# Kernel tuning notes

Measured on AMD Instinct MI355X. Metric: run time of the kernel, lower is better.

Reference implementation:

```python
import jax, jax.numpy as jnp
import numpy as np
from jax import lax

D_MODEL = 200
N_LAYER = 12
NHEADS = 8
HEADDIM = 50
D_STATE = 64
D_INNER = 2 * D_MODEL            # 400
CONV_DIM = D_INNER + 2 * D_STATE  # 528 (ngroups=1)
D_IN_PROJ = 2 * D_INNER + 2 * D_STATE + NHEADS  # 936
D_CONV = 4
EPS = 1e-5


def rmsnorm(x, w):
    v = jnp.mean(jnp.square(x), axis=-1, keepdims=True)
    return x * lax.rsqrt(v + EPS) * w


def groupnorm(x, groups, g, b):
    B, C, H, W = x.shape
    xg = x.reshape(B, groups, C // groups, H, W)
    mu = jnp.mean(xg, axis=(2, 3, 4), keepdims=True)
    var = jnp.mean(jnp.square(xg - mu), axis=(2, 3, 4), keepdims=True)
    xn = ((xg - mu) * lax.rsqrt(var + EPS)).reshape(B, C, H, W)
    return xn * g[:, None, None] + b[:, None, None]


def patch_embed(x, pe_conv_w, proj_in_w, gn_g, gn_b, spec_w):
    b, c, l, d = x.shape
    # time path: 'b c l d' -> (b, 1, c*l, d), conv -> (b, 25, c*l, 8)
    time_x = x.reshape(b, 1, c * l, d)
    t = lax.conv_general_dilated(time_x, proj_in_w, (1, 25), ((0, 0), (24, 24)),
                                 dimension_numbers=('NCHW', 'OIHW', 'NCHW'))
    t = jax.nn.gelu(groupnorm(t, 5, gn_g, gn_b), approximate=False)
    time_emb = t.transpose(0, 2, 1, 3).reshape(b, c, l, D_MODEL)
    # freq path: rfft over patch dim, norm='forward'
    spec = jnp.abs(jnp.fft.rfft(x, axis=-1, norm='forward'))  # (b,c,l,101)
    spec_emb = jnp.einsum('bclf,df->bcld', spec, spec_w)
    patch = time_emb + spec_emb
    # depthwise 7x7 positional conv over (d, c, l)
    pos = lax.conv_general_dilated(patch.transpose(0, 3, 1, 2), pe_conv_w, (1, 1),
                                   ((3, 3), (3, 3)),
                                   dimension_numbers=('NCHW', 'OIHW', 'NCHW'),
                                   feature_group_count=D_MODEL)
    return patch + pos.transpose(0, 2, 3, 1)


def ssd_scan(xh, dt, B, C, A, D):
    # xh: (b,l,h,p)  dt: (b,l,h)  B,C: (b,l,n)  A,D: (h,)
    b, l, h, p = xh.shape

    def step(state, inp):
        x_t, dt_t, B_t, C_t = inp
        dA = jnp.exp(dt_t * A)  # (b,h)
        state = state * dA[:, :, None, None] + \
            (dt_t[:, :, None, None] * x_t[:, :, :, None]) * B_t[:, None, None, :]
        y = jnp.einsum('bhpn,bn->bhp', state, C_t)
        return state, y

    state0 = jnp.zeros((b, h, p, D_STATE), xh.dtype)
    _, ys = lax.scan(step, state0,
                     (xh.transpose(1, 0, 2, 3), dt.transpose(1, 0, 2),
                      B.transpose(1, 0, 2), C.transpose(1, 0, 2)))
    return ys.transpose(1, 0, 2, 3) + xh * D[None, None, :, None]


def mamba2(u, in_w, conv_w, conv_b, dt_bias, A_log, D, gn_w, out_w):
    b, l, _ = u.shape
    zxbcdt = u @ in_w.T  # (b,l,936)
    z = zxbcdt[..., :D_INNER]
    xBC = zxbcdt[..., D_INNER:D_INNER + CONV_DIM]
    dt = jax.nn.softplus(zxbcdt[..., D_INNER + CONV_DIM:] + dt_bias)  # (b,l,8)
    # causal depthwise conv1d, kernel 4
    xc = lax.conv_general_dilated(xBC.transpose(0, 2, 1), conv_w, (1,), ((D_CONV - 1, 0),),
                                  dimension_numbers=('NCH', 'OIH', 'NCH'),
                                  feature_group_count=CONV_DIM)
    xBC = jax.nn.silu((xc + conv_b[:, None]).transpose(0, 2, 1))
    x = xBC[..., :D_INNER].reshape(b, l, NHEADS, HEADDIM)
    Bm = xBC[..., D_INNER:D_INNER + D_STATE]
    Cm = xBC[..., D_INNER + D_STATE:]
    y = ssd_scan(x, dt, Bm, Cm, -jnp.exp(A_log), D).reshape(b, l, D_INNER)
    y = rmsnorm(y * jax.nn.silu(z), gn_w)  # RMSNormGated, norm_before_gate=False
    return y @ out_w.T


@jax.checkpoint
def layer(hidden, residual, norm_w, in_w, conv_w, conv_b, dt_bias, A_log, D, gn_w, out_w):
    residual = hidden + residual
    hidden = mamba2(rmsnorm(residual, norm_w), in_w, conv_w, conv_b, dt_bias, A_log, D, gn_w, out_w)
    return hidden, residual


def forward(x, pe_conv_w, proj_in_w, gn_g, gn_b, spec_w, norm_w, in_proj_w, conv_w, conv_b,
            dt_bias, A_log, D, gnorm_w, out_proj_w, norm_f_w, head_w, head_b):
    b, c, l, d = x.shape
    hidden = patch_embed(x, pe_conv_w, proj_in_w, gn_g, gn_b, spec_w).reshape(b, c * l, d)
    residual = jnp.zeros_like(hidden)
    for i in range(N_LAYER):
        hidden, residual = layer(hidden, residual, norm_w[i], in_proj_w[i], conv_w[i],
                                 conv_b[i], dt_bias[i], A_log[i], D[i], gnorm_w[i], out_proj_w[i])
    hidden = rmsnorm(hidden + residual, norm_f_w).reshape(b, c, l, d)
    return hidden @ head_w.T + head_b


def setup_inputs():
    key = jax.random.key(0)
    ks = jax.random.split(key, 12)
    B, CH, L, P = 16, 19, 30, 200

    def g(k, shape, scale):
        return jax.random.normal(k, shape, jnp.float32) * scale

    dt = jax.random.uniform(ks[8], (N_LAYER, NHEADS), jnp.float32, 1e-3, 0.1)
    return {
        'x': g(ks[0], (B, CH, L, P), 1.0),
        'pe_conv_w': g(ks[1], (D_MODEL, 1, 7, 7), 0.15),
        'proj_in_w': g(ks[2], (25, 1, 1, 49), 0.14),
        'gn_g': jnp.ones(25, jnp.float32),
        'gn_b': jnp.zeros(25, jnp.float32),
        'spec_w': g(ks[3], (D_MODEL, 101), 0.1),
        'norm_w': jnp.ones((N_LAYER, D_MODEL), jnp.float32),
        'in_proj_w': g(ks[4], (N_LAYER, D_IN_PROJ, D_MODEL), 0.07),
        'conv_w': g(ks[5], (N_LAYER, CONV_DIM, 1, D_CONV), 0.4),
        'conv_b': jnp.zeros((N_LAYER, CONV_DIM), jnp.float32),
        'dt_bias': jnp.log(jnp.expm1(dt)),
        'A_log': jnp.log(jax.random.uniform(ks[9], (N_LAYER, NHEADS), jnp.float32, 1.0, 16.0)),
        'D': jnp.ones((N_LAYER, NHEADS), jnp.float32),
        'gnorm_w': jnp.ones((N_LAYER, D_INNER), jnp.float32),
        'out_proj_w': g(ks[6], (N_LAYER, D_MODEL, D_INNER), 0.05),
        'norm_f_w': jnp.ones(D_MODEL, jnp.float32),
        'head_w': g(ks[7], (D_MODEL, D_MODEL), 0.07),
        'head_b': jnp.zeros(D_MODEL, jnp.float32),
    }


def reference(x, pe_conv_w, proj_in_w, gn_g, gn_b, spec_w, norm_w, in_proj_w, conv_w, conv_b,
              dt_bias, A_log, D, gnorm_w, out_proj_w, norm_f_w, head_w, head_b):
    return forward(x, pe_conv_w, proj_in_w, gn_g, gn_b, spec_w, norm_w, in_proj_w, conv_w,
                   conv_b, dt_bias, A_log, D, gnorm_w, out_proj_w, norm_f_w, head_w, head_b)
```

## Files before the change

### kernel.cpp

```cpp
#include <hip/hip_runtime.h>
#include <hip/hip_bf16.h>
#include <math.h>

#define D_MODEL   200
#define N_LAYER   12
#define NHEADS    8
#define HEADDIM   50
#define D_STATE   64
#define D_INNER   400
#define CONV_DIM  528
#define D_IN_PROJ 936
#define D_CONV    4
#define EPS       1e-5f

#define BATCH 16
#define CH    19
#define LLEN  30
#define SEQ   570
#define NTOK  9120
#define NFREQ 101

typedef __attribute__((ext_vector_type(8))) short s8v;
typedef __attribute__((ext_vector_type(4))) float f32x4;

__device__ __forceinline__ short f2bf(float f) {
    unsigned u = __float_as_uint(f);
    u += 0x7FFFu + ((u >> 16) & 1u);
    return (short)(u >> 16);
}

__global__ __launch_bounds__(256) void gemm_bf16(
    const short* __restrict__ A, const short* __restrict__ W,
    const float* __restrict__ bias, float* __restrict__ C,
    int M, int N, int Kp, int accum)
{
    __shared__ __align__(16) short As[128][40];
    __shared__ __align__(16) short Ws[128][40];

    int bm = blockIdx.y * 128;
    int bn = blockIdx.x * 128;
    int tid = threadIdx.x;
    int lane = tid & 63;
    int wv = tid >> 6;
    int wm = wv & 1, wn = wv >> 1;
    int lm = lane & 15, lg = lane >> 4;

    int sr = tid >> 1;
    int sh_ = (tid & 1) * 16;

    f32x4 acc[4][4];
#pragma unroll
    for (int i = 0; i < 4; i++)
#pragma unroll
        for (int j = 0; j < 4; j++) acc[i][j] = (f32x4)0.f;

    for (int k0 = 0; k0 < Kp; k0 += 32) {
        {
            s8v v0 = (s8v)0, v1 = (s8v)0;
            if (bm + sr < M) {
                const short* ga = A + (size_t)(bm + sr) * Kp + k0 + sh_;
                v0 = *(const s8v*)ga;
                v1 = *(const s8v*)(ga + 8);
            }
            *(s8v*)&As[sr][sh_] = v0;
            *(s8v*)&As[sr][sh_ + 8] = v1;
        }
        {
            s8v v0 = (s8v)0, v1 = (s8v)0;
            if (bn + sr < N) {
                const short* gw = W + (size_t)(bn + sr) * Kp + k0 + sh_;
                v0 = *(const s8v*)gw;
                v1 = *(const s8v*)(gw + 8);
            }
            *(s8v*)&Ws[sr][sh_] = v0;
            *(s8v*)&Ws[sr][sh_ + 8] = v1;
        }
        __syncthreads();

        s8v af[4], bf[4];
#pragma unroll
        for (int i = 0; i < 4; i++)
            af[i] = *(const s8v*)&As[wm * 64 + i * 16 + lm][lg * 8];
#pragma unroll
        for (int j = 0; j < 4; j++)
            bf[j] = *(const s8v*)&Ws[wn * 64 + j * 16 + lm][lg * 8];
#pragma unroll
        for (int i = 0; i < 4; i++)
#pragma unroll
            for (int j = 0; j < 4; j++)
                acc[i][j] = __builtin_amdgcn_mfma_f32_16x16x32_bf16(
                    af[i], bf[j], acc[i][j], 0, 0, 0);
        __syncthreads();
    }

#pragma unroll
    for (int j = 0; j < 4; j++) {
        int n = bn + wn * 64 + j * 16 + lm;
        if (n >= N) continue;
        float bv = bias ? bias[n] : 0.f;
#pragma unroll
        for (int i = 0; i < 4; i++) {
            int mbase = bm + wm * 64 + i * 16 + lg * 4;
#pragma unroll
            for (int r = 0; r < 4; r++) {
                int m = mbase + r;
                if (m >= M) continue;
                size_t idx = (size_t)m * N + n;
                float v = acc[i][j][r] + bv;
                if (accum) v += C[idx];
                C[idx] = v;
            }
        }
    }
}

__global__ __launch_bounds__(256) void gemm_nt(
    const float* __restrict__ A, const float* __restrict__ W,
    const float* __restrict__ bias, float* __restrict__ C,
    int M, int N, int K, int accum)
{
    const int BM = 128, BK = 16;
    __shared__ float As[16][BM + 4];
    __shared__ float Ws[16][BM + 4];

    int bm = blockIdx.y * BM;
    int bn = blockIdx.x * BM;
    int tid = threadIdx.x;
    int lr = tid >> 1;
    int lc = (tid & 1) * 8;
    int tx = tid & 15;
    int ty = tid >> 4;

    float acc[8][8];
#pragma unroll
    for (int i = 0; i < 8; i++)
#pragma unroll
        for (int j = 0; j < 8; j++) acc[i][j] = 0.f;

    for (int k0 = 0; k0 < K; k0 += BK) {
#pragma unroll
        for (int i = 0; i < 8; i++) {
            int gr = bm + lr, gk = k0 + lc + i;
            As[lc + i][lr] = (gr < M && gk < K) ? A[(size_t)gr * K + gk] : 0.f;
        }
#pragma unroll
        for (int i = 0; i < 8; i++) {
            int gr = bn + lr, gk = k0 + lc + i;
            Ws[lc + i][lr] = (gr < N && gk < K) ? W[(size_t)gr * K + gk] : 0.f;
        }
        __syncthreads();
#pragma unroll
        for (int kk = 0; kk < BK; kk++) {
            float a[8], bv[8];
#pragma unroll
            for (int i = 0; i < 8; i++) a[i] = As[kk][ty * 8 + i];
#pragma unroll
            for (int j = 0; j < 8; j++) bv[j] = Ws[kk][tx * 8 + j];
#pragma unroll
            for (int i = 0; i < 8; i++)
#pragma unroll
                for (int j = 0; j < 8; j++)
                    acc[i][j] = fmaf(a[i], bv[j], acc[i][j]);
        }
        __syncthreads();
    }

#pragma unroll
    for (int i = 0; i < 8; i++) {
        int gm = bm + ty * 8 + i;
        if (gm >= M) continue;
#pragma unroll
        for (int j = 0; j < 8; j++) {
            int gn = bn + tx * 8 + j;
            if (gn >= N) continue;
            float v = acc[i][j];
            if (bias) v += bias[gn];
            if (accum) v += C[(size_t)gm * N + gn];
            C[(size_t)gm * N + gn] = v;
        }
    }
}

__global__ __launch_bounds__(256) void cast_pad_kernel(
    const float* __restrict__ src, short* __restrict__ dst,
    int R, int K, int Kp)
{
    int idx = blockIdx.x * 256 + threadIdx.x;
    if (idx >= R * Kp) return;
    int r = idx / Kp, k = idx - r * Kp;
    dst[idx] = (k < K) ? f2bf(src[(size_t)r * K + k]) : (short)0;
}

__global__ __launch_bounds__(256) void time_conv_kernel(
    const float* __restrict__ x, const float* __restrict__ pw,
    float* __restrict__ traw)
{
    int br = blockIdx.x;
    __shared__ float xr[200];
    if (threadIdx.x < 200) xr[threadIdx.x] = x[(size_t)br * 200 + threadIdx.x];
    __syncthreads();
    if (threadIdx.x < 200) {
        int oc = threadIdx.x >> 3, j = threadIdx.x & 7;
        int start = j * 25 - 24;
        float acc = 0.f;
#pragma unroll
        for (int k = 0; k < 49; k++) {
            int d = start + k;
            if (d >= 0 && d < 200) acc = fmaf(xr[d], pw[oc * 49 + k], acc);
        }
        int b = br / SEQ, row = br % SEQ;
        traw[(((size_t)b * 25 + oc) * SEQ + row) * 8 + j] = acc;
    }
}

__global__ __launch_bounds__(256) void gn_stats_kernel(
    const float* __restrict__ traw, float* __restrict__ stats)
{
    int bg = blockIdx.x;
    int b = bg / 5, g = bg % 5;
    const float* base = traw + ((size_t)b * 25 + g * 5) * SEQ * 8;
    float s = 0.f, q = 0.f;
    for (int i = threadIdx.x; i < 5 * SEQ * 8; i += 256) {
        float v = base[i];
        s += v; q = fmaf(v, v, q);
    }
    __shared__ float rs[4], rq[4];
    int lane = threadIdx.x & 63, w = threadIdx.x >> 6;
#pragma unroll
    for (int o = 32; o; o >>= 1) { s += __shfl_xor(s, o, 64); q += __shfl_xor(q, o, 64); }
    if (lane == 0) { rs[w] = s; rq[w] = q; }
    __syncthreads();
    if (threadIdx.x == 0) {
        float S = rs[0] + rs[1] + rs[2] + rs[3];
        float Q = rq[0] + rq[1] + rq[2] + rq[3];
        float inv = 1.f / (5.f * SEQ * 8.f);
        float mean = S * inv;
        float var = Q * inv - mean * mean;
        stats[bg * 2] = mean;
        stats[bg * 2 + 1] = rsqrtf(var + EPS);
    }
}

__global__ __launch_bounds__(256) void gn_gelu_kernel(
    const float* __restrict__ traw, const float* __restrict__ stats,
    const float* __restrict__ gn_g, const float* __restrict__ gn_b,
    float* __restrict__ patch)
{
    int idx = blockIdx.x * 256 + threadIdx.x;
    if (idx >= NTOK * 200) return;
    int d = idx % 200;
    int row = (idx / 200) % SEQ;
    int b = idx / (200 * SEQ);
    int oc = d >> 3, j = d & 7;
    float v = traw[(((size_t)b * 25 + oc) * SEQ + row) * 8 + j];
    int g = oc / 5;
    float mean = stats[(b * 5 + g) * 2];
    float rstd = stats[(b * 5 + g) * 2 + 1];
    v = (v - mean) * rstd * gn_g[oc] + gn_b[oc];
    float ge = 0.5f * v * (1.f + erff(v * 0.70710678118654752f));
    patch[idx] = ge;
}
// ... 275 lines not shown
                tok = (tid >= 66) ? 1 : 0;
                fidx = tid - tok * 66;
                int tq = t + 2 + tok; if (tq > SEQ - 1) tq = SEQ - 1;
                int g = (fidx < 50) ? (50 * bz + fidx) : (fidx + 50);
                rx = ((const float4*)(xBC + (size_t)(b * SEQ + tq) * CONV_DIM))[g];
            } else if (tid < 140) {
                int e = tid - 132, tk = e >> 2, hd = e & 3;
                int tq = t + 2 + tk; if (tq > SEQ - 1) tq = SEQ - 1;
                rdt = dtb[(size_t)(b * SEQ + tq) * NHEADS + bz * 4 + hd];
            }
        }
#pragma unroll
        for (int k = 0; k < 2; k++) {
            float dtv = sh[buf][k][264 + hl];
            float xp  = (p < HEADDIM) ? sh[buf][k][hl * HEADDIM + p] : 0.f;
            float dA = __expf(dtv * A);
            float u  = dtv * xp;
            pacc *= dA;
            const float4* B4 = (const float4*)&sh[buf][k][200];
#pragma unroll
            for (int n4 = 0; n4 < 16; n4++) {
                float4 bq = B4[n4];
                s[4 * n4 + 0] = fmaf(s[4 * n4 + 0], dA, u * bq.x);
                s[4 * n4 + 1] = fmaf(s[4 * n4 + 1], dA, u * bq.y);
                s[4 * n4 + 2] = fmaf(s[4 * n4 + 2], dA, u * bq.z);
                s[4 * n4 + 3] = fmaf(s[4 * n4 + 3], dA, u * bq.w);
            }
        }
        if (pf) {
            if (tid < 132) *(float4*)&sh[nb][tok][fidx * 4] = rx;
            else if (tid < 140) { int e = tid - 132; sh[nb][e >> 2][264 + (e & 3)] = rdt; }
        }
        __syncthreads();
    }

    if (rem) {
        int buf = npairs & 1;
        float dtv = sh[buf][0][264 + hl];
        float xp  = (p < HEADDIM) ? sh[buf][0][hl * HEADDIM + p] : 0.f;
        float dA = __expf(dtv * A);
        float u  = dtv * xp;
        pacc *= dA;
        const float4* B4 = (const float4*)&sh[buf][0][200];
#pragma unroll
        for (int n4 = 0; n4 < 16; n4++) {
            float4 bq = B4[n4];
            s[4 * n4 + 0] = fmaf(s[4 * n4 + 0], dA, u * bq.x);
            s[4 * n4 + 1] = fmaf(s[4 * n4 + 1], dA, u * bq.y);
            s[4 * n4 + 2] = fmaf(s[4 * n4 + 2], dA, u * bq.z);
            s[4 * n4 + 3] = fmaf(s[4 * n4 + 3], dA, u * bq.w);
        }
    }

    if (p < HEADDIM) {
        float* Sb = Sbuf + ((size_t)((b * NHEADS + h) * nchunk + c)) * (HEADDIM * 64)
                    + p * 64;
#pragma unroll
        for (int n4 = 0; n4 < 16; n4++)
            ((float4*)Sb)[n4] = make_float4(s[4 * n4], s[4 * n4 + 1],
                                            s[4 * n4 + 2], s[4 * n4 + 3]);
    }
    if (p == 0) Pd[(b * NHEADS + h) * nchunk + c] = pacc;
}

__global__ __launch_bounds__(512) void ssd_state_kernel(
    const float* __restrict__ xBC, const float* __restrict__ dtb,
    const float* __restrict__ A_log, float* __restrict__ Sbuf,
    float* __restrict__ Pd, int layer, int lchunk, int nchunk)
{
    int b = blockIdx.x, c = blockIdx.y;
    int tid = threadIdx.x;
    int h = tid >> 6, p = tid & 63;
    float A = -expf(A_log[layer * NHEADS + h]);

    __shared__ float sh[2][544];
    int t0 = c * lchunk, tend = t0 + lchunk;

    {
        const float* base = xBC + (size_t)(b * SEQ + t0) * CONV_DIM;
        sh[0][tid] = base[tid];
        if (tid < 24) {
            int e2 = 512 + tid;
            sh[0][e2] = (e2 < 528) ? base[e2]
                                   : dtb[(size_t)(b * SEQ + t0) * NHEADS + (e2 - 528)];
        }
    }
    __syncthreads();

    float s[64];
#pragma unroll
    for (int n = 0; n < 64; n++) s[n] = 0.f;
    float pacc = 1.f;

    for (int t = t0; t < tend; t++) {
        int cur = (t - t0) & 1, nxt = cur ^ 1;
        float pf0 = 0.f, pf1 = 0.f;
        if (t + 1 < tend) {
            const float* base = xBC + (size_t)(b * SEQ + t + 1) * CONV_DIM;
            pf0 = base[tid];
            if (tid < 24) {
                int e2 = 512 + tid;
                pf1 = (e2 < 528) ? base[e2]
                                 : dtb[(size_t)(b * SEQ + t + 1) * NHEADS + (e2 - 528)];
            }
        }
        float dtv = sh[cur][528 + h];
        float xp  = (p < HEADDIM) ? sh[cur][h * HEADDIM + p] : 0.f;
        float dA = __expf(dtv * A);
        float u  = dtv * xp;
        pacc *= dA;
        const float4* B4 = (const float4*)&sh[cur][D_INNER];
#pragma unroll
        for (int n4 = 0; n4 < 16; n4++) {
            float4 bq = B4[n4];
            s[4 * n4 + 0] = fmaf(s[4 * n4 + 0], dA, u * bq.x);
            s[4 * n4 + 1] = fmaf(s[4 * n4 + 1], dA, u * bq.y);
            s[4 * n4 + 2] = fmaf(s[4 * n4 + 2], dA, u * bq.z);
            s[4 * n4 + 3] = fmaf(s[4 * n4 + 3], dA, u * bq.w);
        }
        if (t + 1 < tend) {
            sh[nxt][tid] = pf0;
            if (tid < 24) sh[nxt][512 + tid] = pf1;
        }
        __syncthreads();
    }

    if (p < HEADDIM) {
        float* Sb = Sbuf + ((size_t)((b * NHEADS + h) * nchunk + c)) * (HEADDIM * 64)
                    + p * 64;
#pragma unroll
        for (int n4 = 0; n4 < 16; n4++)
            ((float4*)Sb)[n4] = make_float4(s[4 * n4], s[4 * n4 + 1],
                                            s[4 * n4 + 2], s[4 * n4 + 3]);
    }
    if (p == 0) Pd[(b * NHEADS + h) * nchunk + c] = pacc;
}

__global__ __launch_bounds__(256) void ssd_scan2b_kernel(
    float* __restrict__ Sbuf, const float* __restrict__ Pd, int nchunk)
{
    int bh = blockIdx.x;
    int e = blockIdx.y * 256 + threadIdx.x;
    if (e >= HEADDIM * 64) return;
    float* base = Sbuf + (size_t)bh * nchunk * (HEADDIM * 64) + e;
    const float* pd = Pd + bh * nchunk;
    float cur = 0.f;
    for (int c = 0; c < nchunk; c++) {
        float l = base[(size_t)c * (HEADDIM * 64)];
        base[(size_t)c * (HEADDIM * 64)] = cur;
        cur = fmaf(pd[c], cur, l);
    }
}

__global__ __launch_bounds__(512) void ssd_out_fused3_kernel(
    const float* __restrict__ xBC, const float* __restrict__ dtb,
    const float* __restrict__ zxbcdt, const float* __restrict__ A_log,
    const float* __restrict__ Dv, const float* __restrict__ Sbuf,
    const float* __restrict__ gw, short* __restrict__ ybf,
    int layer, int lchunk, int nchunk)
{
    int b = blockIdx.x, c = blockIdx.y;
    int tid = threadIdx.x;
    int h = tid >> 6, p = tid & 63;
    float A = -expf(A_log[layer * NHEADS + h]);
    float Dh = Dv[layer * NHEADS + h];
    float gval = (p < HEADDIM) ? gw[(size_t)layer * D_INNER + h * HEADDIM + p] : 0.f;

    __shared__ __align__(16) float sh[2][2][536];
    __shared__ __align__(16) float shz[2][2][400];
    __shared__ float red[2][2][8];
    int t0 = c * lchunk;
    int npairs = lchunk >> 1, rem = lchunk & 1;

    {
        if (tid < 264) {
            int wch = (tid >= 132) ? 1 : 0;
            int fidx = tid - wch * 132;
            int tq = t0 + wch;
            float4 v = ((const float4*)(xBC + (size_t)(b * SEQ + tq) * CONV_DIM))[fidx];
            *(float4*)&sh[0][wch][fidx * 4] = v;
        } else if (tid < 280) {
            int e = tid - 264, tok = e >> 3, hd = e & 7;
            sh[0][tok][528 + hd] = dtb[(size_t)(b * SEQ + t0 + tok) * NHEADS + hd];
        } else if (tid < 480) {
            int wch = (tid >= 380) ? 1 : 0;
            int fidx = tid - 280 - wch * 100;
            int tq = t0 + wch;
            float4 v = ((const float4*)(zxbcdt + (size_t)(b * SEQ + tq) * D_IN_PROJ))[fidx];
            *(float4*)&shz[0][wch][fidx * 4] = v;
        }
    }

    float s[64];
    if (p < HEADDIM) {
        const float* Sb = Sbuf + ((size_t)((b * NHEADS + h) * nchunk + c)) * (HEADDIM * 64)
                          + p * 64;
#pragma unroll
        for (int n4 = 0; n4 < 16; n4++) {
            float4 v = ((const float4*)Sb)[n4];
            s[4 * n4] = v.x; s[4 * n4 + 1] = v.y; s[4 * n4 + 2] = v.z; s[4 * n4 + 3] = v.w;
        }
    } else {
#pragma unroll
        for (int n = 0; n < 64; n++) s[n] = 0.f;
    }
    __syncthreads();

    for (int i = 0; i < npairs; i++) {
        int t = t0 + 2 * i;
        int buf = i & 1, nb = buf ^ 1;
        bool pf = (2 * i + 2 < lchunk);
        float4 rx, rz;
        float rdt = 0.f;
        int wch = 0, fidx = 0, zwch = 0, zfidx = 0;
        if (pf) {
            if (tid < 264) {
                wch = (tid >= 132) ? 1 : 0;
                fidx = tid - wch * 132;
                int tq = t + 2 + wch; if (tq > SEQ - 1) tq = SEQ - 1;
                rx = ((const float4*)(xBC + (size_t)(b * SEQ + tq) * CONV_DIM))[fidx];
            } else if (tid < 280) {
                int e = tid - 264, tok = e >> 3, hd = e & 7;
                int tq = t + 2 + tok; if (tq > SEQ - 1) tq = SEQ - 1;
                rdt = dtb[(size_t)(b * SEQ + tq) * NHEADS + hd];
            } else if (tid < 480) {
                zwch = (tid >= 380) ? 1 : 0;
                zfidx = tid - 280 - zwch * 100;
                int tq = t + 2 + zwch; if (tq > SEQ - 1) tq = SEQ - 1;
                rz = ((const float4*)(zxbcdt + (size_t)(b * SEQ + tq) * D_IN_PROJ))[zfidx];
            }
        }
        float g0 = 0.f, g1 = 0.f;
#pragma unroll
        for (int k = 0; k < 2; k++) {
            float dtv = sh[buf][k][528 + h];
            float xp  = (p < HEADDIM) ? sh[buf][k][h * HEADDIM + p] : 0.f;
            float dA = __expf(dtv * A);
            float u  = dtv * xp;
            const float4* B4 = (const float4*)&sh[buf][k][D_INNER];
            const float4* C4 = (const float4*)&sh[buf][k][D_INNER + D_STATE];
            float y0 = 0.f, y1 = 0.f, y2 = 0.f, y3 = 0.f;
#pragma unroll
            for (int n4 = 0; n4 < 16; n4++) {
                float4 bq = B4[n4];
                float4 cq = C4[n4];
                float t0v = fmaf(s[4 * n4 + 0], dA, u * bq.x);
                float t1v = fmaf(s[4 * n4 + 1], dA, u * bq.y);
                float t2v = fmaf(s[4 * n4 + 2], dA, u * bq.z);
                float t3v = fmaf(s[4 * n4 + 3], dA, u * bq.w);
                s[4 * n4 + 0] = t0v; s[4 * n4 + 1] = t1v;
                s[4 * n4 + 2] = t2v; s[4 * n4 + 3] = t3v;
                y0 = fmaf(t0v, cq.x, y0);
                y1 = fmaf(t1v, cq.y, y1);
                y2 = fmaf(t2v, cq.z, y2);
                y3 = fmaf(t3v, cq.w, y3);
            }
            if (p < HEADDIM) {
                float yv = fmaf(xp, Dh, (y0 + y1) + (y2 + y3));
                float zv = shz[buf][k][h * HEADDIM + p];
                float g = yv * (zv / (1.f + __expf(-zv)));
                if (k == 0) g0 = g; else g1 = g;
            }
        }
        float gs0 = g0 * g0, gs1 = g1 * g1;
#pragma unroll
        for (int o = 32; o; o >>= 1) {
            gs0 += __shfl_xor(gs0, o, 64);
            gs1 += __shfl_xor(gs1, o, 64);
        }
        if (p == 0) { red[buf][0][h] = gs0; red[buf][1][h] = gs1; }
        if (pf) {
            if (tid < 264) *(float4*)&sh[nb][wch][fidx * 4] = rx;
            else if (tid < 280) { int e = tid - 264; sh[nb][e >> 3][528 + (e & 7)] = rdt; }
            else if (tid < 480) *(float4*)&shz[nb][zwch][zfidx * 4] = rz;
        }
        __syncthreads();
        float tot0 = (red[buf][0][0] + red[buf][0][1]) + (red[buf][0][2] + red[buf][0][3]) +
                     (red[buf][0][4] + red[buf][0][5]) + (red[buf][0][6] + red[buf][0][7]);
        float tot1 = (red[buf][1][0] + red[buf][1][1]) + (red[buf][1][2] + red[buf][1][3]) +
                     (red[buf][1][4] + red[buf][1][5]) + (red[buf][1][6] + red[buf][1][7]);
        float rstd0 = rsqrtf(tot0 * (1.f / D_INNER) + EPS);
        float rstd1 = rsqrtf(tot1 * (1.f / D_INNER) + EPS);
        size_t row0 = (size_t)(b * SEQ + t) * 416;
        size_t row1 = (size_t)(b * SEQ + t + 1) * 416;
        if (p < HEADDIM) {
            ybf[row0 + h * HEADDIM + p] = f2bf(g0 * rstd0 * gval);
            ybf[row1 + h * HEADDIM + p] = f2bf(g1 * rstd1 * gval);
        } else {
            int widx = h * 14 + (p - HEADDIM);
            if (widx < 16) {
                ybf[row0 + 400 + widx] = 0;
                ybf[row1 + 400 + widx] = 0;
            }
        }
    }

    if (rem) {
        int buf = npairs & 1;
        int t = t0 + lchunk - 1;
        float g0 = 0.f;
        {
            float dtv = sh[buf][0][528 + h];
            float xp  = (p < HEADDIM) ? sh[buf][0][h * HEADDIM + p] : 0.f;
            float dA = __expf(dtv * A);
            float u  = dtv * xp;
            const float4* B4 = (const float4*)&sh[buf][0][D_INNER];
            const float4* C4 = (const float4*)&sh[buf][0][D_INNER + D_STATE];
            float y0 = 0.f, y1 = 0.f, y2 = 0.f, y3 = 0.f;
#pragma unroll
            for (int n4 = 0; n4 < 16; n4++) {
                float4 bq = B4[n4];
                float4 cq = C4[n4];
                float t0v = fmaf(s[4 * n4 + 0], dA, u * bq.x);
                float t1v = fmaf(s[4 * n4 + 1], dA, u * bq.y);
                float t2v = fmaf(s[4 * n4 + 2], dA, u * bq.z);
                float t3v = fmaf(s[4 * n4 + 3], dA, u * bq.w);
                s[4 * n4 + 0] = t0v; s[4 * n4 + 1] = t1v;
                s[4 * n4 + 2] = t2v; s[4 * n4 + 3] = t3v;
                y0 = fmaf(t0v, cq.x, y0);
                y1 = fmaf(t1v, cq.y, y1);
                y2 = fmaf(t2v, cq.z, y2);
                y3 = fmaf(t3v, cq.w, y3);
            }
            if (p < HEADDIM) {
                float yv = fmaf(xp, Dh, (y0 + y1) + (y2 + y3));
                float zv = shz[buf][0][h * HEADDIM + p];
                g0 = yv * (zv / (1.f + __expf(-zv)));
            }
        }
        float gs0 = g0 * g0;
#pragma unroll
        for (int o = 32; o; o >>= 1) gs0 += __shfl_xor(gs0, o, 64);
        if (p == 0) red[buf][0][h] = gs0;
        __syncthreads();
        float tot0 = (red[buf][0][0] + red[buf][0][1]) + (red[buf][0][2] + red[buf][0][3]) +
                     (red[buf][0][4] + red[buf][0][5]) + (red[buf][0][6] + red[buf][0][7]);
        float rstd0 = rsqrtf(tot0 * (1.f / D_INNER) + EPS);
        size_t row0 = (size_t)(b * SEQ + t) * 416;
        if (p < HEADDIM) {
            ybf[row0 + h * HEADDIM + p] = f2bf(g0 * rstd0 * gval);
        } else {
            int widx = h * 14 + (p - HEADDIM);
            if (widx < 16) ybf[row0 + 400 + widx] = 0;
        }
    }
}

__global__ __launch_bounds__(512) void ssd_out_kernel(
    const float* __restrict__ xBC, const float* __restrict__ dtb,
    const float* __restrict__ A_log, const float* __restrict__ Dv,
    const float* __restrict__ Sbuf, float* __restrict__ y,
    int layer, int lchunk, int nchunk)
{
    int b = blockIdx.x, c = blockIdx.y;
    int tid = threadIdx.x;
    int h = tid >> 6, p = tid & 63;
    float A = -expf(A_log[layer * NHEADS + h]);
    float Dh = Dv[layer * NHEADS + h];

    __shared__ float sh[2][544];
    int t0 = c * lchunk, tend = t0 + lchunk;

    {
        const float* base = xBC + (size_t)(b * SEQ + t0) * CONV_DIM;
        sh[0][tid] = base[tid];
        if (tid < 24) {
            int e2 = 512 + tid;
            sh[0][e2] = (e2 < 528) ? base[e2]
                                   : dtb[(size_t)(b * SEQ + t0) * NHEADS + (e2 - 528)];
        }
    }

    float s[64];
    if (p < HEADDIM) {
        const float* Sb = Sbuf + ((size_t)((b * NHEADS + h) * nchunk + c)) * (HEADDIM * 64)
                          + p * 64;
#pragma unroll
        for (int n4 = 0; n4 < 16; n4++) {
            float4 v = ((const float4*)Sb)[n4];
            s[4 * n4] = v.x; s[4 * n4 + 1] = v.y; s[4 * n4 + 2] = v.z; s[4 * n4 + 3] = v.w;
        }
    } else {
#pragma unroll
        for (int n = 0; n < 64; n++) s[n] = 0.f;
    }
    __syncthreads();

    for (int t = t0; t < tend; t++) {
        int cur = (t - t0) & 1, nxt = cur ^ 1;
        float pf0 = 0.f, pf1 = 0.f;
        if (t + 1 < tend) {
            const float* base = xBC + (size_t)(b * SEQ + t + 1) * CONV_DIM;
            pf0 = base[tid];
            if (tid < 24) {
                int e2 = 512 + tid;
                pf1 = (e2 < 528) ? base[e2]
                                 : dtb[(size_t)(b * SEQ + t + 1) * NHEADS + (e2 - 528)];
            }
        }
        float dtv = sh[cur][528 + h];
        float xp  = (p < HEADDIM) ? sh[cur][h * HEADDIM + p] : 0.f;
        float dA = __expf(dtv * A);
        float u  = dtv * xp;
        const float4* B4 = (const float4*)&sh[cur][D_INNER];
        const float4* C4 = (const float4*)&sh[cur][D_INNER + D_STATE];
        float y0 = 0.f, y1 = 0.f, y2 = 0.f, y3 = 0.f;
#pragma unroll
        for (int n4 = 0; n4 < 16; n4++) {
            float4 bq = B4[n4];
            float4 cq = C4[n4];
            float t0v = fmaf(s[4 * n4 + 0], dA, u * bq.x);
            float t1v = fmaf(s[4 * n4 + 1], dA, u * bq.y);
            float t2v = fmaf(s[4 * n4 + 2], dA, u * bq.z);
            float t3v = fmaf(s[4 * n4 + 3], dA, u * bq.w);
            s[4 * n4 + 0] = t0v; s[4 * n4 + 1] = t1v;
            s[4 * n4 + 2] = t2v; s[4 * n4 + 3] = t3v;
            y0 = fmaf(t0v, cq.x, y0);
            y1 = fmaf(t1v, cq.y, y1);
            y2 = fmaf(t2v, cq.z, y2);
            y3 = fmaf(t3v, cq.w, y3);
        }
        if (p < HEADDIM) {
            float yv = (y0 + y1) + (y2 + y3);
            y[(size_t)(b * SEQ + t) * D_INNER + h * HEADDIM + p] = fmaf(xp, Dh, yv);
        }
        if (t + 1 < tend) {
            sh[nxt][tid] = pf0;
            if (tid < 24) sh[nxt][512 + tid] = pf1;
        }
        __syncthreads();
    }
}

__global__ __launch_bounds__(256) void gate_norm_kernel(
    float* __restrict__ y, const float* __restrict__ zxbcdt,
    const float* __restrict__ gw, short* __restrict__ ybf, int layer)
{
    int m = blockIdx.x;
    __shared__ float buf[D_INNER];
    __shared__ float red[4];
    const float* z = zxbcdt + (size_t)m * D_IN_PROJ;
    float* yr = y + (size_t)m * D_INNER;
    const float* gwl = gw + (size_t)layer * D_INNER;
    float ss = 0.f;
    for (int k = threadIdx.x; k < D_INNER; k += 256) {
        float zv = z[k];
        float sz = zv / (1.f + expf(-zv));
        float g = yr[k] * sz;
        buf[k] = g;
        ss = fmaf(g, g, ss);
    }
    int lane = threadIdx.x & 63, w = threadIdx.x >> 6;
#pragma unroll
    for (int o = 32; o; o >>= 1) ss += __shfl_xor(ss, o, 64);
    if (lane == 0) red[w] = ss;
    __syncthreads();
    float tot = red[0] + red[1] + red[2] + red[3];
    float rstd = rsqrtf(tot * (1.f / D_INNER) + EPS);
    for (int k = threadIdx.x; k < 416; k += 256) {
        if (k < D_INNER) {
            float v = buf[k] * rstd * gwl[k];
            yr[k] = v;
            if (ybf) ybf[(size_t)m * 416 + k] = f2bf(v);
        } else if (ybf) {
            ybf[(size_t)m * 416 + k] = 0;
        }
    }
}

extern "C" void kernel_launch(void* const* d_in, const int* in_sizes, int n_in,
                              void* d_out, int out_size, void* d_ws, size_t ws_size,
                              hipStream_t stream)
{
    const float* x         = (const float*)d_in[0];
    const float* pe_conv_w = (const float*)d_in[1];
    const float* proj_in_w = (const float*)d_in[2];
    const float* gn_g      = (const float*)d_in[3];
    const float* gn_b      = (const float*)d_in[4];
    const float* spec_w    = (const float*)d_in[5];
    const float* norm_w    = (const float*)d_in[6];
    const float* in_proj_w = (const float*)d_in[7];
    const float* conv_w    = (const float*)d_in[8];
    const float* conv_b    = (const float*)d_in[9];
    const float* dt_bias   = (const float*)d_in[10];
    const float* A_log     = (const float*)d_in[11];
    const float* Dv        = (const float*)d_in[12];
    const float* gnorm_w   = (const float*)d_in[13];
    const float* out_proj_w= (const float*)d_in[14];
    const float* norm_f_w  = (const float*)d_in[15];
    const float* head_w    = (const float*)d_in[16];
    const float* head_b    = (const float*)d_in[17];
    float* out = (float*)d_out;
    float* ws  = (float*)d_ws;

    const size_t needA = 27929344ull * sizeof(float);
    int fast = (ws_size >= needA) ? 1 : 0;

    int nchunk, lchunk;
    float *residual = ws, *hidden = ws + 1824000;
    float *zxbcdt, *xBC, *dtb, *Sbuf, *Pd;
    float *ubuf = nullptr, *ybuf = nullptr;
    short *w_in_bf = nullptr, *w_out_bf = nullptr, *w_head_bf = nullptr,
          *w_spec_bf = nullptr, *csmat_bf = nullptr, *x_bf = nullptr,
          *ubuf_bf = nullptr, *ybuf_bf = nullptr, *magb_bf = nullptr;

    if (fast) {
        nchunk = 15; lchunk = 38;
        zxbcdt = ws + 3648000;
        xBC    = ws + 12184320;
        dtb    = ws + 16999680;
        Sbuf   = ws + 17072640;
        Pd     = ws + 23216640;
        short* pool = (short*)(ws + 23218560);
        w_in_bf   = pool;
        w_out_bf  = pool + 2515968;
        w_head_bf = pool + 3514368;
        w_spec_bf = pool + 3559168;
        ubuf_bf   = pool + 3584768;
        ybuf_bf   = pool + 5627648;
        csmat_bf  = (short*)(Sbuf + 4000000);
        x_bf      = (short*)(Sbuf + 4100000);
        magb_bf   = (short*)(Sbuf + 5200000);
    } else {
        nchunk = 6; lchunk = 95;
        ubuf   = ws + 3648000;
        zxbcdt = ws + 5472000;
        xBC    = ws + 14008320;
        dtb    = ws + 18823680;
        ybuf   = ws + 18896640;
        Sbuf   = ws + 1824000;
        Pd     = ws + 5470000;
    }

    float* traw  = fast ? Sbuf : ybuf;
    float* patch = zxbcdt;
    float* csout = fast ? (Sbuf + 2000000) : (xBC + 50000);
    float* csmat = xBC;
    float* magb  = fast ? nullptr : (xBC + 2000000);
    float* stats = dtb;

    if (fast) {
        cast_pad_kernel<<<(12 * 936 * 224 + 255) / 256, 256, 0, stream>>>(
            in_proj_w, w_in_bf, 12 * 936, 200, 224);
        cast_pad_kernel<<<(12 * 200 * 416 + 255) / 256, 256, 0, stream>>>(
            out_proj_w, w_out_bf, 12 * 200, 400, 416);
        cast_pad_kernel<<<(200 * 224 + 255) / 256, 256, 0, stream>>>(
            head_w, w_head_bf, 200, 200, 224);
        cast_pad_kernel<<<(200 * 128 + 255) / 256, 256, 0, stream>>>(
            spec_w, w_spec_bf, 200, 101, 128);
        cast_pad_kernel<<<(9120 * 224 + 255) / 256, 256, 0, stream>>>(
            x, x_bf, 9120, 200, 224);
        dft_init_bf_kernel<<<(202 * 224 + 255) / 256, 256, 0, stream>>>(csmat_bf);
    } else {
        dft_init_kernel<<<(202 * 200 + 255) / 256, 256, 0, stream>>>(csmat);
    }

    time_conv_kernel<<<NTOK, 256, 0, stream>>>(x, proj_in_w, traw);
    gn_stats_kernel<<<80, 256, 0, stream>>>(traw, stats);
    gn_gelu_kernel<<<(NTOK * 200 + 255) / 256, 256, 0, stream>>>(traw, stats, gn_g, gn_b, patch);
    if (fast) {
        gemm_bf16<<<dim3(2, 72), 256, 0, stream>>>(x_bf, csmat_bf, nullptr, csout,
                                                   NTOK, 202, 224, 0);
        mag_bf_kernel<<<(NTOK * 128 + 255) / 256, 256, 0, stream>>>(csout, magb_bf);
        gemm_bf16<<<dim3(2, 72), 256, 0, stream>>>(magb_bf, w_spec_bf, nullptr, patch,
                                                   NTOK, 200, 128, 1);
    } else {
        gemm_nt<<<dim3(2, 72), 256, 0, stream>>>(x, csmat, nullptr, csout, NTOK, 202, 200, 0);
        mag_kernel<<<(NTOK * NFREQ + 255) / 256, 256, 0, stream>>>(csout, magb);
        gemm_nt<<<dim3(2, 72), 256, 0, stream>>>(magb, spec_w, nullptr, patch,
                                                 NTOK, 200, NFREQ, 1);
    }
    pe_conv3_kernel<<<dim3(16, 13, 5), 256, 0, stream>>>(patch, pe_conv_w, hidden);

    for (int i = 0; i < N_LAYER; i++) {
        if (fast) {
            norm_dt_kernel<<<NTOK, 256, 0, stream>>>(hidden, residual, norm_w + i * 200,
                                                     ubuf_bf, in_proj_w, dt_bias, dtb,
                                                     i, (i == 0) ? 1 : 0);
            gemm_bf16<<<dim3(8, 72), 256, 0, stream>>>(
                ubuf_bf, w_in_bf + (size_t)i * 936 * 224, nullptr, zxbcdt,
                NTOK, D_IN_PROJ, 224, 0);
        } else {
            add_rmsnorm_kernel<<<NTOK, 64, 0, stream>>>(hidden, residual, norm_w + i * 200,
                                                        ubuf, nullptr, (i == 0) ? 1 : 0);
            dt_gemv_kernel<<<NTOK / 4, 256, 0, stream>>>(ubuf, in_proj_w, dt_bias, dtb, i);
            gemm_nt<<<dim3(8, 72), 256, 0, stream>>>(
                ubuf, in_proj_w + (size_t)i * D_IN_PROJ * 200, nullptr, zxbcdt,
                NTOK, D_IN_PROJ, 200, 0);
        }
        dtconv2_kernel<<<dim3(16, 72), 256, 0, stream>>>(zxbcdt, conv_w, conv_b, xBC, i);
        {
            dim3 g(BATCH, nchunk);
            if (fast) {
                ssd_state4_kernel<<<dim3(BATCH, nchunk, 2), 256, 0, stream>>>(
                    xBC, dtb, A_log, Sbuf, Pd, i, lchunk, nchunk);
                ssd_scan2b_kernel<<<dim3(BATCH * NHEADS, 13), 256, 0, stream>>>(Sbuf, Pd, nchunk);
                ssd_out_fused3_kernel<<<g, 512, 0, stream>>>(
                    xBC, dtb, zxbcdt, A_log, Dv, Sbuf, gnorm_w, ybuf_bf, i, lchunk, nchunk);
                gemm_bf16<<<dim3(2, 72), 256, 0, stream>>>(
                    ybuf_bf, w_out_bf + (size_t)i * 200 * 416, nullptr, hidden,
                    NTOK, 200, 416, 0);
            } else {
                ssd_state_kernel<<<g, 512, 0, stream>>>(xBC, dtb, A_log, Sbuf, Pd,
                                                        i, lchunk, nchunk);
                ssd_scan2b_kernel<<<dim3(BATCH * NHEADS, 13), 256, 0, stream>>>(Sbuf, Pd, nchunk);
                ssd_out_kernel<<<g, 512, 0, stream>>>(xBC, dtb, A_log, Dv, Sbuf, ybuf,
                                                      i, lchunk, nchunk);
                gate_norm_kernel<<<NTOK, 256, 0, stream>>>(ybuf, zxbcdt, gnorm_w, nullptr, i);
                gemm_nt<<<dim3(2, 72), 256, 0, stream>>>(
                    ybuf, out_proj_w + (size_t)i * 200 * D_INNER, nullptr, hidden,
                    NTOK, 200, D_INNER, 0);
            }
        }
    }

    add_rmsnorm_kernel<<<NTOK, 64, 0, stream>>>(hidden, residual, norm_f_w,
                                                fast ? nullptr : ubuf,
                                                fast ? ubuf_bf : nullptr, 0);
    if (fast) {
        gemm_bf16<<<dim3(2, 72), 256, 0, stream>>>(ubuf_bf, w_head_bf, head_b, out,
                                                   NTOK, 200, 224, 0);
    } else {
        gemm_nt<<<dim3(2, 72), 256, 0, stream>>>(ubuf, head_w, head_b, out,
                                                 NTOK, 200, 200, 0);
    }
}
```

Measured before the change: 2.490 ms.

## Split SSD output kernel across head halves and defer group-norm scale to GEMM

The fused SSD output kernel now runs with two blocks per (batch, chunk), each covering 4 heads with 256 threads, which doubles block count for better occupancy. Because a block no longer sees every head, it writes per-half sums of squares. A small rstd kernel combines the halves, and the out-projection GEMM applies the per-row rstd in its epilogue. The odd-length remainder path is dropped, so this assumes lchunk is even. It also adds one extra kernel launch per layer.

```diff
diff --git a/kernel.cpp b/kernel.cpp
--- a/kernel.cpp
+++ b/kernel.cpp
@@ -31,8 +31,8 @@
 
 __global__ __launch_bounds__(256) void gemm_bf16(
     const short* __restrict__ A, const short* __restrict__ W,
-    const float* __restrict__ bias, float* __restrict__ C,
-    int M, int N, int Kp, int accum)
+    const float* __restrict__ bias, const float* __restrict__ rowscale,
+    float* __restrict__ C, int M, int N, int Kp, int accum)
 {
     __shared__ __align__(16) short As[128][40];
     __shared__ __align__(16) short Ws[128][40];
@@ -106,7 +106,9 @@
                 int m = mbase + r;
                 if (m >= M) continue;
                 size_t idx = (size_t)m * N + n;
-                float v = acc[i][j][r] + bv;
+                float v = acc[i][j][r];
+                if (rowscale) v *= rowscale[m];
+                v += bv;
                 if (accum) v += C[idx];
                 C[idx] = v;
             }
@@ -688,42 +690,43 @@
     }
 }
 
-__global__ __launch_bounds__(512) void ssd_out_fused3_kernel(
+__global__ __launch_bounds__(256) void ssd_out5_kernel(
     const float* __restrict__ xBC, const float* __restrict__ dtb,
     const float* __restrict__ zxbcdt, const float* __restrict__ A_log,
     const float* __restrict__ Dv, const float* __restrict__ Sbuf,
     const float* __restrict__ gw, short* __restrict__ ybf,
-    int layer, int lchunk, int nchunk)
-{
-    int b = blockIdx.x, c = blockIdx.y;
+    float* __restrict__ ssq, int layer, int lchunk, int nchunk)
+{
+    int b = blockIdx.x, c = blockIdx.y, bz = blockIdx.z;
     int tid = threadIdx.x;
-    int h = tid >> 6, p = tid & 63;
+    int hl = tid >> 6, p = tid & 63;
+    int h = bz * 4 + hl;
     float A = -expf(A_log[layer * NHEADS + h]);
     float Dh = Dv[layer * NHEADS + h];
     float gval = (p < HEADDIM) ? gw[(size_t)layer * D_INNER + h * HEADDIM + p] : 0.f;
 
-    __shared__ __align__(16) float sh[2][2][536];
-    __shared__ __align__(16) float shz[2][2][400];
-    __shared__ float red[2][2][8];
+    __shared__ __align__(16) float sh[2][2][336];
+    __shared__ __align__(16) float shz[2][2][200];
+    __shared__ float red[2][2][4];
     int t0 = c * lchunk;
-    int npairs = lchunk >> 1, rem = lchunk & 1;
+    int npairs = lchunk >> 1;
 
     {
-        if (tid < 264) {
-            int wch = (tid >= 132) ? 1 : 0;
-            int fidx = tid - wch * 132;
-            int tq = t0 + wch;
-            float4 v = ((const float4*)(xBC + (size_t)(b * SEQ + tq) * CONV_DIM))[fidx];
-            *(float4*)&sh[0][wch][fidx * 4] = v;
-        } else if (tid < 280) {
-            int e = tid - 264, tok = e >> 3, hd = e & 7;
-            sh[0][tok][528 + hd] = dtb[(size_t)(b * SEQ + t0 + tok) * NHEADS + hd];
-        } else if (tid < 480) {
-            int wch = (tid >= 380) ? 1 : 0;
-            int fidx = tid - 280 - wch * 100;
-            int tq = t0 + wch;
-            float4 v = ((const float4*)(zxbcdt + (size_t)(b * SEQ + tq) * D_IN_PROJ))[fidx];
-            *(float4*)&shz[0][wch][fidx * 4] = v;
+        if (tid < 164) {
+            int tok = (tid >= 82) ? 1 : 0;
+            int fidx = tid - tok * 82;
+            int g = (fidx < 50) ? (50 * bz + fidx) : (fidx + 50);
+            float4 v = ((const float4*)(xBC + (size_t)(b * SEQ + t0 + tok) * CONV_DIM))[g];
+            *(float4*)&sh[0][tok][fidx * 4] = v;
+        } else if (tid < 172) {
+            int e = tid - 164, tok = e >> 2, hd = e & 3;
+            sh[0][tok][328 + hd] = dtb[(size_t)(b * SEQ + t0 + tok) * NHEADS + bz * 4 + hd];
+        }
+        if (tid < 100) {
+            int tok = (tid >= 50) ? 1 : 0;
+            int fz = tid - tok * 50;
+            float4 v = ((const float4*)(zxbcdt + (size_t)(b * SEQ + t0 + tok) * D_IN_PROJ))[50 * bz + fz];
+            *(float4*)&shz[0][tok][fz * 4] = v;
         }
     }
 
@@ -748,33 +751,35 @@
         bool pf = (2 * i + 2 < lchunk);
         float4 rx, rz;
         float rdt = 0.f;
-        int wch = 0, fidx = 0, zwch = 0, zfidx = 0;
+        int xtok = 0, xf = 0, ztok = 0, zf = 0;
         if (pf) {
-            if (tid < 264) {
-                wch = (tid >= 132) ? 1 : 0;
-                fidx = tid - wch * 132;
-                int tq = t + 2 + wch; if (tq > SEQ - 1) tq = SEQ - 1;
-                rx = ((const float4*)(xBC + (size_t)(b * SEQ + tq) * CONV_DIM))[fidx];
-            } else if (tid < 280) {
-                int e = tid - 264, tok = e >> 3, hd = e & 7;
-                int tq = t + 2 + tok; if (tq > SEQ - 1) tq = SEQ - 1;
-                rdt = dtb[(size_t)(b * SEQ + tq) * NHEADS + hd];
-            } else if (tid < 480) {
-                zwch = (tid >= 380) ? 1 : 0;
-                zfidx = tid - 280 - zwch * 100;
-                int tq = t + 2 + zwch; if (tq > SEQ - 1) tq = SEQ - 1;
-                rz = ((const float4*)(zxbcdt + (size_t)(b * SEQ + tq) * D_IN_PROJ))[zfidx];
+            if (tid < 164) {
+                xtok = (tid >= 82) ? 1 : 0;
+                xf = tid - xtok * 82;
+                int tq = t + 2 + xtok; if (tq > SEQ - 1) tq = SEQ - 1;
+                int g = (xf < 50) ? (50 * bz + xf) : (xf + 50);
+                rx = ((const float4*)(xBC + (size_t)(b * SEQ + tq) * CONV_DIM))[g];
+            } else if (tid < 172) {
+                int e = tid - 164, tk = e >> 2, hd = e & 3;
+                int tq = t + 2 + tk; if (tq > SEQ - 1) tq = SEQ - 1;
+                rdt = dtb[(size_t)(b * SEQ + tq) * NHEADS + bz * 4 + hd];
+            }
+            if (tid < 100) {
+                ztok = (tid >= 50) ? 1 : 0;
+                zf = tid - ztok * 50;
+                int tq = t + 2 + ztok; if (tq > SEQ - 1) tq = SEQ - 1;
+                rz = ((const float4*)(zxbcdt + (size_t)(b * SEQ + tq) * D_IN_PROJ))[50 * bz + zf];
             }
         }
         float g0 = 0.f, g1 = 0.f;
 #pragma unroll
         for (int k = 0; k < 2; k++) {
-            float dtv = sh[buf][k][528 + h];
-            float xp  = (p < HEADDIM) ? sh[buf][k][h * HEADDIM + p] : 0.f;
+            float dtv = sh[buf][k][328 + hl];
+            float xp  = (p < HEADDIM) ? sh[buf][k][hl * HEADDIM + p] : 0.f;
             float dA = __expf(dtv * A);
             float u  = dtv * xp;
-            const float4* B4 = (const float4*)&sh[buf][k][D_INNER];
-            const float4* C4 = (const float4*)&sh[buf][k][D_INNER + D_STATE];
+            const float4* B4 = (const float4*)&sh[buf][k][200];
+            const float4* C4 = (const float4*)&sh[buf][k][264];
             float y0 = 0.f, y1 = 0.f, y2 = 0.f, y3 = 0.f;
 #pragma unroll
             for (int n4 = 0; n4 < 16; n4++) {
@@ -793,35 +798,16 @@
             }
             if (p < HEADDIM) {
                 float yv = fmaf(xp, Dh, (y0 + y1) + (y2 + y3));
-                float zv = shz[buf][k][h * HEADDIM + p];
+                float zv = shz[buf][k][hl * HEADDIM + p];
                 float g = yv * (zv / (1.f + __expf(-zv)));
                 if (k == 0) g0 = g; else g1 = g;
             }
         }
-        float gs0 = g0 * g0, gs1 = g1 * g1;
-#pragma unroll
-        for (int o = 32; o; o >>= 1) {
-            gs0 += __shfl_xor(gs0, o, 64);
-            gs1 += __shfl_xor(gs1, o, 64);
-        }
-        if (p == 0) { red[buf][0][h] = gs0; red[buf][1][h] = gs1; }
-        if (pf) {
-            if (tid < 264) *(float4*)&sh[nb][wch][fidx * 4] = rx;
-            else if (tid < 280) { int e = tid - 264; sh[nb][e >> 3][528 + (e & 7)] = rdt; }
-            else if (tid < 480) *(float4*)&shz[nb][zwch][zfidx * 4] = rz;
-        }
-        __syncthreads();
-        float tot0 = (red[buf][0][0] + red[buf][0][1]) + (red[buf][0][2] + red[buf][0][3]) +
-                     (red[buf][0][4] + red[buf][0][5]) + (red[buf][0][6] + red[buf][0][7]);
-        float tot1 = (red[buf][1][0] + red[buf][1][1]) + (red[buf][1][2] + red[buf][1][3]) +
-                     (red[buf][1][4] + red[buf][1][5]) + (red[buf][1][6] + red[buf][1][7]);
-        float rstd0 = rsqrtf(tot0 * (1.f / D_INNER) + EPS);
-        float rstd1 = rsqrtf(tot1 * (1.f / D_INNER) + EPS);
         size_t row0 = (size_t)(b * SEQ + t) * 416;
-        size_t row1 = (size_t)(b * SEQ + t + 1) * 416;
+        size_t row1 = row0 + 416;
         if (p < HEADDIM) {
-            ybf[row0 + h * HEADDIM + p] = f2bf(g0 * rstd0 * gval);
-            ybf[row1 + h * HEADDIM + p] = f2bf(g1 * rstd1 * gval);
+            ybf[row0 + h * HEADDIM + p] = f2bf(g0 * gval);
+            ybf[row1 + h * HEADDIM + p] = f2bf(g1 * gval);
         } else {
             int widx = h * 14 + (p - HEADDIM);
             if (widx < 16) {
@@ -829,57 +815,34 @@
                 ybf[row1 + 400 + widx] = 0;
             }
         }
-    }
-
-    if (rem) {
-        int buf = npairs & 1;
-        int t = t0 + lchunk - 1;
-        float g0 = 0.f;
-        {
-            float dtv = sh[buf][0][528 + h];
-            float xp  = (p < HEADDIM) ? sh[buf][0][h * HEADDIM + p] : 0.f;
-            float dA = __expf(dtv * A);
-            float u  = dtv * xp;
-            const float4* B4 = (const float4*)&sh[buf][0][D_INNER];
-            const float4* C4 = (const float4*)&sh[buf][0][D_INNER + D_STATE];
-            float y0 = 0.f, y1 = 0.f, y2 = 0.f, y3 = 0.f;
-#pragma unroll
-            for (int n4 = 0; n4 < 16; n4++) {
-                float4 bq = B4[n4];
-                float4 cq = C4[n4];
-                float t0v = fmaf(s[4 * n4 + 0], dA, u * bq.x);
-                float t1v = fmaf(s[4 * n4 + 1], dA, u * bq.y);
-                float t2v = fmaf(s[4 * n4 + 2], dA, u * bq.z);
-                float t3v = fmaf(s[4 * n4 + 3], dA, u * bq.w);
-                s[4 * n4 + 0] = t0v; s[4 * n4 + 1] = t1v;
-                s[4 * n4 + 2] = t2v; s[4 * n4 + 3] = t3v;
-                y0 = fmaf(t0v, cq.x, y0);
-                y1 = fmaf(t1v, cq.y, y1);
-                y2 = fmaf(t2v, cq.z, y2);
-                y3 = fmaf(t3v, cq.w, y3);
-            }
-            if (p < HEADDIM) {
-                float yv = fmaf(xp, Dh, (y0 + y1) + (y2 + y3));
-                float zv = shz[buf][0][h * HEADDIM + p];
-                g0 = yv * (zv / (1.f + __expf(-zv)));
-            }
-        }
-        float gs0 = g0 * g0;
-#pragma unroll
-        for (int o = 32; o; o >>= 1) gs0 += __shfl_xor(gs0, o, 64);
-        if (p == 0) red[buf][0][h] = gs0;
+        float gs0 = g0 * g0, gs1 = g1 * g1;
+#pragma unroll
+        for (int o = 32; o; o >>= 1) {
+            gs0 += __shfl_xor(gs0, o, 64);
+            gs1 += __shfl_xor(gs1, o, 64);
+        }
+        if (p == 0) { red[buf][0][hl] = gs0; red[buf][1][hl] = gs1; }
+        if (pf) {
+            if (tid < 164) *(float4*)&sh[nb][xtok][xf * 4] = rx;
+            else if (tid < 172) { int e = tid - 164; sh[nb][e >> 2][328 + (e & 3)] = rdt; }
+            if (tid < 100) *(float4*)&shz[nb][ztok][zf * 4] = rz;
+        }
         __syncthreads();
-        float tot0 = (red[buf][0][0] + red[buf][0][1]) + (red[buf][0][2] + red[buf][0][3]) +
-                     (red[buf][0][4] + red[buf][0][5]) + (red[buf][0][6] + red[buf][0][7]);
-        float rstd0 = rsqrtf(tot0 * (1.f / D_INNER) + EPS);
-        size_t row0 = (size_t)(b * SEQ + t) * 416;
-        if (p < HEADDIM) {
-            ybf[row0 + h * HEADDIM + p] = f2bf(g0 * rstd0 * gval);
-        } else {
-            int widx = h * 14 + (p - HEADDIM);
-            if (widx < 16) ybf[row0 + 400 + widx] = 0;
-        }
-    }
+        if (tid == 0) {
+            ssq[(size_t)(b * SEQ + t) * 2 + bz] =
+                (red[buf][0][0] + red[buf][0][1]) + (red[buf][0][2] + red[buf][0][3]);
+            ssq[(size_t)(b * SEQ + t + 1) * 2 + bz] =
+                (red[buf][1][0] + red[buf][1][1]) + (red[buf][1][2] + red[buf][1][3]);
+        }
+    }
+}
+
+__global__ __launch_bounds__(256) void rstd_kernel(
+    const float* __restrict__ ssq, float* __restrict__ rstdb)
+{
+    int m = blockIdx.x * 256 + threadIdx.x;
+    if (m >= NTOK) return;
+    rstdb[m] = rsqrtf((ssq[2 * m] + ssq[2 * m + 1]) * (1.f / D_INNER) + EPS);
 }
 
 __global__ __launch_bounds__(512) void ssd_out_kernel(
@@ -1029,13 +992,13 @@
     float* out = (float*)d_out;
     float* ws  = (float*)d_ws;
 
-    const size_t needA = 27929344ull * sizeof(float);
+    const size_t needA = 27956704ull * sizeof(float);
     int fast = (ws_size >= needA) ? 1 : 0;
 
     int nchunk, lchunk;
     float *residual = ws, *hidden = ws + 1824000;
     float *zxbcdt, *xBC, *dtb, *Sbuf, *Pd;
-    float *ubuf = nullptr, *ybuf = nullptr;
+    float *ubuf = nullptr, *ybuf = nullptr, *ssq = nullptr, *rstdb = nullptr;
     short *w_in_bf = nullptr, *w_out_bf = nullptr, *w_head_bf = nullptr,
           *w_spec_bf = nullptr, *csmat_bf = nullptr, *x_bf = nullptr,
           *ubuf_bf = nullptr, *ybuf_bf = nullptr, *magb_bf = nullptr;
@@ -1054,6 +1017,8 @@
         w_spec_bf = pool + 3559168;
         ubuf_bf   = pool + 3584768;
         ybuf_bf   = pool + 5627648;
+        ssq       = ws + 27929344;
+        rstdb     = ws + 27947584;
         csmat_bf  = (short*)(Sbuf + 4000000);
         x_bf      = (short*)(Sbuf + 4100000);
         magb_bf   = (short*)(Sbuf + 5200000);
@@ -1095,10 +1060,10 @@
     gn_stats_kernel<<<80, 256, 0, stream>>>(traw, stats);
     gn_gelu_kernel<<<(NTOK * 200 + 255) / 256, 256, 0, stream>>>(traw, stats, gn_g, gn_b, patch);
     if (fast) {
-        gemm_bf16<<<dim3(2, 72), 256, 0, stream>>>(x_bf, csmat_bf, nullptr, csout,
+        gemm_bf16<<<dim3(2, 72), 256, 0, stream>>>(x_bf, csmat_bf, nullptr, nullptr, csout,
                                                    NTOK, 202, 224, 0);
         mag_bf_kernel<<<(NTOK * 128 + 255) / 256, 256, 0, stream>>>(csout, magb_bf);
-        gemm_bf16<<<dim3(2, 72), 256, 0, stream>>>(magb_bf, w_spec_bf, nullptr, patch,
+        gemm_bf16<<<dim3(2, 72), 256, 0, stream>>>(magb_bf, w_spec_bf, nullptr, nullptr, patch,
                                                    NTOK, 200, 128, 1);
     } else {
         gemm_nt<<<dim3(2, 72), 256, 0, stream>>>(x, csmat, nullptr, csout, NTOK, 202, 200, 0);
@@ -1114,7 +1079,7 @@
                                                      ubuf_bf, in_proj_w, dt_bias, dtb,
                                                      i, (i == 0) ? 1 : 0);
             gemm_bf16<<<dim3(8, 72), 256, 0, stream>>>(
-                ubuf_bf, w_in_bf + (size_t)i * 936 * 224, nullptr, zxbcdt,
+                ubuf_bf, w_in_bf + (size_t)i * 936 * 224, nullptr, nullptr, zxbcdt,
                 NTOK, D_IN_PROJ, 224, 0);
         } else {
             add_rmsnorm_kernel<<<NTOK, 64, 0, stream>>>(hidden, residual, norm_w + i * 200,
@@ -1131,10 +1096,12 @@
                 ssd_state4_kernel<<<dim3(BATCH, nchunk, 2), 256, 0, stream>>>(
                     xBC, dtb, A_log, Sbuf, Pd, i, lchunk, nchunk);
                 ssd_scan2b_kernel<<<dim3(BATCH * NHEADS, 13), 256, 0, stream>>>(Sbuf, Pd, nchunk);
-                ssd_out_fused3_kernel<<<g, 512, 0, stream>>>(
-                    xBC, dtb, zxbcdt, A_log, Dv, Sbuf, gnorm_w, ybuf_bf, i, lchunk, nchunk);
+                ssd_out5_kernel<<<dim3(BATCH, nchunk, 2), 256, 0, stream>>>(
+                    xBC, dtb, zxbcdt, A_log, Dv, Sbuf, gnorm_w, ybuf_bf, ssq,
+                    i, lchunk, nchunk);
+                rstd_kernel<<<(NTOK + 255) / 256, 256, 0, stream>>>(ssq, rstdb);
                 gemm_bf16<<<dim3(2, 72), 256, 0, stream>>>(
-                    ybuf_bf, w_out_bf + (size_t)i * 200 * 416, nullptr, hidden,
+                    ybuf_bf, w_out_bf + (size_t)i * 200 * 416, nullptr, rstdb, hidden,
                     NTOK, 200, 416, 0);
             } else {
                 ssd_state_kernel<<<g, 512, 0, stream>>>(xBC, dtb, A_log, Sbuf, Pd,
@@ -1154,7 +1121,7 @@
                                                 fast ? nullptr : ubuf,
                                                 fast ? ubuf_bf : nullptr, 0);
     if (fast) {
-        gemm_bf16<<<dim3(2, 72), 256, 0, stream>>>(ubuf_bf, w_head_bf, head_b, out,
+        gemm_bf16<<<dim3(2, 72), 256, 0, stream>>>(ubuf_bf, w_head_bf, head_b, nullptr, out,
                                                    NTOK, 200, 224, 0);
     } else {
         gemm_nt<<<dim3(2, 72), 256, 0, stream>>>(ubuf, head_w, head_b, out,
```

Measured after the change: 2.433 ms. 1.02x faster.
